# Performance work log

Hardware: AMD Instinct MI355X
Metric: run time of the kernel (lower is better)

## Reference

```python
import jax, jax.numpy as jnp
import numpy as np

B, N, H, F, G = 16, 192, 128, 128, 50


def setup_inputs() -> dict:
    key = jax.random.key(0)
    ks = jax.random.split(key, 12)
    s = lambda fan_in: 1.0 / np.sqrt(fan_in)
    inp = {
        "features": jax.random.normal(ks[0], (B, N, H), jnp.float32),
        "rbf": jax.random.uniform(ks[1], (B, N, N, G), jnp.float32),
        "neighbour_mask": jax.random.randint(ks[2], (B, N, N), 0, 2, jnp.int32),
        # dense_rbf: Linear(G,F) -> Softplus -> Linear(F,F)
        "W_rbf1": jax.random.uniform(ks[3], (G, F), jnp.float32, -s(G), s(G)),
        "b_rbf1": jnp.zeros((F,), jnp.float32),
        "W_rbf2": jax.random.uniform(ks[4], (F, F), jnp.float32, -s(F), s(F)),
        "b_rbf2": jnp.zeros((F,), jnp.float32),
        # dense_f: Linear(H,F)
        "W_f": jax.random.uniform(ks[5], (H, F), jnp.float32, -s(H), s(H)),
        "b_f": jnp.zeros((F,), jnp.float32),
        # dense_out: Linear(F,H) -> Softplus -> Linear(H,H)
        "W_o1": jax.random.uniform(ks[6], (F, H), jnp.float32, -s(F), s(F)),
        "b_o1": jnp.zeros((H,), jnp.float32),
        "W_o2": jax.random.uniform(ks[7], (H, H), jnp.float32, -s(H), s(H)),
        "b_o2": jnp.zeros((H,), jnp.float32),
    }
    return inp


def reference(features, rbf, neighbour_mask, W_rbf1, b_rbf1, W_rbf2, b_rbf2,
              W_f, b_f, W_o1, b_o1, W_o2, b_o2):
    # filter network on RBF expansion: [B,N,N,G] -> [B,N,N,F]
    fw = jax.nn.softplus(rbf @ W_rbf1 + b_rbf1) @ W_rbf2 + b_rbf2
    # neighbor features: [B,N,H] -> [B,1,N,F] (broadcast over central-atom axis)
    nf = (features @ W_f + b_f)[:, None, :, :]
    mask = neighbour_mask.astype(fw.dtype)[..., None]  # [B,N,N,1]
    # messages [B,N,N,F], masked sum over neighbor axis -> [B,N,F]
    aggregated = jnp.sum(fw * nf * mask, axis=2)
    out = jax.nn.softplus(aggregated @ W_o1 + b_o1) @ W_o2 + b_o2  # [B,N,H]
    return features + out
```

## Files before the change

kernel.cpp:

```cpp
#include <hip/hip_runtime.h>
#include <hip/hip_bf16.h>


typedef __bf16 bf16_t;
typedef __bf16 bf16x8 __attribute__((ext_vector_type(8)));
typedef float  f32x4  __attribute__((ext_vector_type(4)));

constexpr int kB = 16, kN = 192, kH = 128, kF = 128, kG = 50;
constexpr int kRows = kB * kN;
constexpr int kHsPitch = 136;

__device__ __forceinline__ float ldf(const void* p, int i, bool bfm) {
  return bfm ? (float)((const bf16_t*)p)[i] : ((const float*)p)[i];
}

__device__ __forceinline__ float softplus_f(float x) {
  float t = __logf(1.f + __expf(fminf(x, 20.f)));
  return x > 20.f ? x : t;
}

__global__ __launch_bounds__(256) void detect_kernel(const unsigned int* __restrict__ rbf_w,
                                                     int* __restrict__ flag) {
  __shared__ int c_hi, c_zero;
  const int t = threadIdx.x;
  if (t == 0) { c_hi = 0; c_zero = 0; }
  __syncthreads();
  unsigned int w = rbf_w[(size_t)t * 40003u];
  unsigned int lo = w & 0xFFFFu;
  if (((lo >> 7) & 0xFFu) >= 128u) atomicAdd(&c_hi, 1);
  if (lo == 0u) atomicAdd(&c_zero, 1);
  __syncthreads();
  if (t == 0) *flag = (c_hi == 0 && c_zero < 200) ? 1 : 0;
}

__global__ __launch_bounds__(256) void prep_kernel(const void* __restrict__ W1,
                                                   const void* __restrict__ W2,
                                                   const int* __restrict__ flag,
                                                   bf16_t* __restrict__ w1t,
                                                   bf16_t* __restrict__ w2t) {
  const bool bfm = *flag != 0;
  int idx = blockIdx.x * 256 + threadIdx.x;
  if (idx < 128 * 64) {
    int n = idx >> 6, k = idx & 63;
    w1t[idx] = (k < kG) ? (bf16_t)ldf(W1, k * kF + n, bfm) : (bf16_t)0.f;
  } else if (idx < 128 * 64 + 128 * 128) {
    int id2 = idx - 128 * 64;
    int n = id2 >> 7, k = id2 & 127;
    w2t[id2] = (bf16_t)ldf(W2, k * kF + n, bfm);
  }
}

__global__ __launch_bounds__(128) void nf_kernel(const void* __restrict__ features,
                                                 const void* __restrict__ Wf,
                                                 const void* __restrict__ bfv,
                                                 const int* __restrict__ flag,
                                                 float* __restrict__ nf) {
  const bool bfm = *flag != 0;
  int row = blockIdx.x, f = threadIdx.x;
  __shared__ float s_x[kH];
  s_x[f] = ldf(features, row * kH + f, bfm);
  __syncthreads();
  float acc = ldf(bfv, f, bfm);
#pragma unroll 8
  for (int k = 0; k < kH; ++k) acc = fmaf(s_x[k], ldf(Wf, k * kF + f, bfm), acc);
  nf[row * kF + f] = acc;
}

__global__ __launch_bounds__(256) void main_kernel(
    const void* __restrict__ rbf, const int* __restrict__ nmask,
    const void* __restrict__ b1p, const void* __restrict__ b2p,
    const bf16_t* __restrict__ w1t, const bf16_t* __restrict__ w2t,
    const float* __restrict__ nf, const int* __restrict__ flag,
    float* __restrict__ agg) {
  __shared__ bf16_t s_hs[kN * kHsPitch];
  __shared__ float  s_mask[kN];
  __shared__ float  s_agg[kF];

  const bool bfm = *flag != 0;
  const int bi = blockIdx.x;
  const int b  = bi / kN;
  const int t  = threadIdx.x;
  const int wave = t >> 6, lane = t & 63;
  const int n16 = lane & 15, q = lane >> 4;
  const int m0w = wave * 48;

  for (int idx = t; idx < kN; idx += 256) s_mask[idx] = (float)nmask[bi * kN + idx];
  if (t < kF) s_agg[t] = 0.f;

  f32x4 acc[3][8];
#pragma unroll
  for (int mt = 0; mt < 3; ++mt)
#pragma unroll
    for (int nt = 0; nt < 8; ++nt)
#pragma unroll
      for (int r = 0; r < 4; ++r) acc[mt][nt][r] = 0.f;

  const size_t rbase = (size_t)bi * (kN * kG);
#pragma unroll
  for (int ks = 0; ks < 2; ++ks) {
    bf16x8 afr[3];
#pragma unroll
    for (int mt = 0; mt < 3; ++mt) {
      const int j  = m0w + mt * 16 + n16;
      const int kb = ks * 32 + q * 8;
      if (bfm) {
        const bf16_t* rp = (const bf16_t*)rbf + rbase + (size_t)j * kG;
#pragma unroll
        for (int i = 0; i < 8; ++i) {
          int k = kb + i;
          afr[mt][i] = (k < kG) ? rp[k] : (bf16_t)0.f;
        }
      } else {
        const float* rp = (const float*)rbf + rbase + (size_t)j * kG;
#pragma unroll
        for (int i = 0; i < 8; ++i) {
          int k = kb + i;
          afr[mt][i] = (bf16_t)((k < kG) ? rp[k] : 0.f);
        }
      }
    }
#pragma unroll
    for (int nt = 0; nt < 8; ++nt) {
      bf16x8 bfr = *(const bf16x8*)(w1t + (nt * 16 + n16) * 64 + ks * 32 + q * 8);
#pragma unroll
      for (int mt = 0; mt < 3; ++mt)
        acc[mt][nt] = __builtin_amdgcn_mfma_f32_16x16x32_bf16(afr[mt], bfr, acc[mt][nt], 0, 0, 0);
    }
  }

#pragma unroll
  for (int nt = 0; nt < 8; ++nt) {
    const int col = nt * 16 + n16;
    const float bb = ldf(b1p, col, bfm);
#pragma unroll
    for (int mt = 0; mt < 3; ++mt) {
      const int jb = m0w + mt * 16 + q * 4;
#pragma unroll
      for (int r = 0; r < 4; ++r)
        s_hs[(jb + r) * kHsPitch + col] = (bf16_t)softplus_f(acc[mt][nt][r] + bb);
    }
  }
  __syncthreads();

#pragma unroll
  for (int mt = 0; mt < 3; ++mt)
#pragma unroll
    for (int nt = 0; nt < 8; ++nt)
#pragma unroll
      for (int r = 0; r < 4; ++r) acc[mt][nt][r] = 0.f;

#pragma unroll
  for (int ks = 0; ks < 4; ++ks) {
    bf16x8 afr[3];
#pragma unroll
    for (int mt = 0; mt < 3; ++mt)
      afr[mt] = *(const bf16x8*)(s_hs + (m0w + mt * 16 + n16) * kHsPitch + ks * 32 + q * 8);
#pragma unroll
    for (int nt = 0; nt < 8; ++nt) {
      bf16x8 bfr = *(const bf16x8*)(w2t + (nt * 16 + n16) * 128 + ks * 32 + q * 8);
#pragma unroll
      for (int mt = 0; mt < 3; ++mt)
        acc[mt][nt] = __builtin_amdgcn_mfma_f32_16x16x32_bf16(afr[mt], bfr, acc[mt][nt], 0, 0, 0);
    }
  }

#pragma unroll
  for (int nt = 0; nt < 8; ++nt) {
    const int f = nt * 16 + n16;
    const float b2v = ldf(b2p, f, bfm);
    float p = 0.f;
#pragma unroll
    for (int mt = 0; mt < 3; ++mt) {
      const int jb = m0w + mt * 16 + q * 4;
#pragma unroll
      for (int r = 0; r < 4; ++r) {
        const int j = jb + r;
        const float m   = s_mask[j];
        const float nfv = nf[((size_t)b * kN + j) * kF + f];
        p = fmaf(m * (acc[mt][nt][r] + b2v), nfv, p);
      }
    }
    atomicAdd(&s_agg[f], p);
  }
  __syncthreads();
  if (t < kF) agg[(size_t)bi * kF + t] = s_agg[t];
}

__global__ __launch_bounds__(128) void out_kernel(
    const float* __restrict__ agg, const void* __restrict__ features,
    const void* __restrict__ Wo1, const void* __restrict__ bo1,
    const void* __restrict__ Wo2, const void* __restrict__ bo2,
    const int* __restrict__ flag, void* __restrict__ out) {
  const bool bfm = *flag != 0;
  int row = blockIdx.x, h = threadIdx.x;
  __shared__ float s_a[kF], s_t[kH];
  s_a[h] = agg[row * kF + h];
  __syncthreads();
  float a1 = ldf(bo1, h, bfm);
#pragma unroll 8
  for (int k = 0; k < kF; ++k) a1 = fmaf(s_a[k], ldf(Wo1, k * kH + h, bfm), a1);
  s_t[h] = softplus_f(a1);
  __syncthreads();
  float a2 = ldf(bo2, h, bfm);
#pragma unroll 8
  for (int k = 0; k < kH; ++k) a2 = fmaf(s_t[k], ldf(Wo2, k * kH + h, bfm), a2);
  float res = ldf(features, row * kH + h, bfm) + a2;
  if (bfm) ((bf16_t*)out)[row * kH + h] = (bf16_t)res;
  else     ((float*)out)[row * kH + h]  = res;
}

extern "C" void kernel_launch(void* const* d_in, const int* in_sizes, int n_in,
                              void* d_out, int out_size, void* d_ws, size_t ws_size,
                              hipStream_t stream) {
  const void* features = d_in[0];
  const void* rbf      = d_in[1];
  const int*  nmask    = (const int*)d_in[2];
  const void* W1  = d_in[3];
  const void* b1  = d_in[4];
  const void* W2  = d_in[5];
  const void* b2  = d_in[6];
  const void* Wf  = d_in[7];
  const void* bfv = d_in[8];
  const void* Wo1 = d_in[9];
  const void* bo1 = d_in[10];
  const void* Wo2 = d_in[11];
  const void* bo2 = d_in[12];

  char* ws = (char*)d_ws;
  float*  nf   = (float*)ws;
  float*  agg  = (float*)(ws + 1572864);
  bf16_t* w1t  = (bf16_t*)(ws + 3145728);
  bf16_t* w2t  = (bf16_t*)(ws + 3162112);
  int*    flag = (int*)(ws + 3194880);

  detect_kernel<<<1, 256, 0, stream>>>((const unsigned int*)rbf, flag);
  prep_kernel<<<96, 256, 0, stream>>>(W1, W2, flag, w1t, w2t);
  nf_kernel<<<kRows, 128, 0, stream>>>(features, Wf, bfv, flag, nf);
  main_kernel<<<kRows, 256, 0, stream>>>(rbf, nmask, b1, b2, w1t, w2t, nf, flag, agg);
  out_kernel<<<kRows, 128, 0, stream>>>(agg, features, Wo1, bo1, Wo2, bo2, flag, d_out);
}
```

Measured before the change: 353.8 us.

## Stage rbf through LDS with vector loads and fuse kernels into two launches

Drops the bf16 detection kernel and the dtype flag, so every path assumes fp32 inputs. Merges the weight-transpose prep and nf projection into one launch, and folds the output MLP into the end of the main kernel. The main kernel now loads each block's rbf tile with coalesced float4 loads, converts it to bf16 in shared memory, and builds MFMA fragments from there instead of doing strided scalar global loads. This removes launch overhead, the agg round trip and uncoalesced rbf reads, at the cost of more LDS use and a serial tail MLP run by half the threads.

```diff
diff --git a/kernel.cpp b/kernel.cpp
--- a/kernel.cpp
+++ b/kernel.cpp
@@ -6,77 +6,70 @@
 typedef __bf16 bf16x8 __attribute__((ext_vector_type(8)));
 typedef float  f32x4  __attribute__((ext_vector_type(4)));
 
-constexpr int kB = 16, kN = 192, kH = 128, kF = 128, kG = 50;
-constexpr int kRows = kB * kN;
+constexpr int kN = 192, kH = 128, kF = 128, kG = 50;
+constexpr int kRows = 16 * kN;
 constexpr int kHsPitch = 136;
-
-__device__ __forceinline__ float ldf(const void* p, int i, bool bfm) {
-  return bfm ? (float)((const bf16_t*)p)[i] : ((const float*)p)[i];
-}
+constexpr int kRbfRowB = kG * 2;
+constexpr int kRbfF32PerBlk = kN * kG;
+constexpr int kRbfVec4 = kRbfF32PerBlk / 4;
 
 __device__ __forceinline__ float softplus_f(float x) {
   float t = __logf(1.f + __expf(fminf(x, 20.f)));
   return x > 20.f ? x : t;
 }
 
-__global__ __launch_bounds__(256) void detect_kernel(const unsigned int* __restrict__ rbf_w,
-                                                     int* __restrict__ flag) {
-  __shared__ int c_hi, c_zero;
-  const int t = threadIdx.x;
-  if (t == 0) { c_hi = 0; c_zero = 0; }
-  __syncthreads();
-  unsigned int w = rbf_w[(size_t)t * 40003u];
-  unsigned int lo = w & 0xFFFFu;
-  if (((lo >> 7) & 0xFFu) >= 128u) atomicAdd(&c_hi, 1);
-  if (lo == 0u) atomicAdd(&c_zero, 1);
-  __syncthreads();
-  if (t == 0) *flag = (c_hi == 0 && c_zero < 200) ? 1 : 0;
-}
-
-__global__ __launch_bounds__(256) void prep_kernel(const void* __restrict__ W1,
-                                                   const void* __restrict__ W2,
-                                                   const int* __restrict__ flag,
-                                                   bf16_t* __restrict__ w1t,
-                                                   bf16_t* __restrict__ w2t) {
-  const bool bfm = *flag != 0;
-  int idx = blockIdx.x * 256 + threadIdx.x;
-  if (idx < 128 * 64) {
-    int n = idx >> 6, k = idx & 63;
-    w1t[idx] = (k < kG) ? (bf16_t)ldf(W1, k * kF + n, bfm) : (bf16_t)0.f;
-  } else if (idx < 128 * 64 + 128 * 128) {
-    int id2 = idx - 128 * 64;
-    int n = id2 >> 7, k = id2 & 127;
-    w2t[id2] = (bf16_t)ldf(W2, k * kF + n, bfm);
-  }
-}
-
-__global__ __launch_bounds__(128) void nf_kernel(const void* __restrict__ features,
-                                                 const void* __restrict__ Wf,
-                                                 const void* __restrict__ bfv,
-                                                 const int* __restrict__ flag,
-                                                 float* __restrict__ nf) {
-  const bool bfm = *flag != 0;
-  int row = blockIdx.x, f = threadIdx.x;
+__global__ __launch_bounds__(64) void pre_kernel(
+    const float* __restrict__ features, const float* __restrict__ Wf,
+    const float* __restrict__ bfv, const float* __restrict__ W1,
+    const float* __restrict__ W2, float* __restrict__ nf,
+    bf16_t* __restrict__ w1t, bf16_t* __restrict__ w2t) {
+  const int lane = threadIdx.x;
+  if (blockIdx.x >= kRows) {
+    if (blockIdx.x == kRows) {
+      for (int i = lane; i < 128 * 64; i += 64) {
+        int n = i >> 6, k = i & 63;
+        w1t[i] = (k < kG) ? (bf16_t)W1[k * kF + n] : (bf16_t)0.f;
+      }
+    } else {
+      for (int i = lane; i < 128 * 128; i += 64) {
+        int n = i >> 7, k = i & 127;
+        w2t[i] = (bf16_t)W2[k * kF + n];
+      }
+    }
+    return;
+  }
+  const int row = blockIdx.x;
   __shared__ float s_x[kH];
-  s_x[f] = ldf(features, row * kH + f, bfm);
-  __syncthreads();
-  float acc = ldf(bfv, f, bfm);
+  const float* fr = features + (size_t)row * kH;
+  s_x[lane] = fr[lane];
+  s_x[64 + lane] = fr[64 + lane];
+  __syncthreads();
+  float a0 = bfv[lane], a1 = bfv[64 + lane];
 #pragma unroll 8
-  for (int k = 0; k < kH; ++k) acc = fmaf(s_x[k], ldf(Wf, k * kF + f, bfm), acc);
-  nf[row * kF + f] = acc;
+  for (int k = 0; k < kH; ++k) {
+    float xk = s_x[k];
+    a0 = fmaf(xk, Wf[k * kF + lane], a0);
+    a1 = fmaf(xk, Wf[k * kF + 64 + lane], a1);
+  }
+  float* nr = nf + (size_t)row * kF;
+  nr[lane] = a0;
+  nr[64 + lane] = a1;
 }
 
 __global__ __launch_bounds__(256) void main_kernel(
-    const void* __restrict__ rbf, const int* __restrict__ nmask,
-    const void* __restrict__ b1p, const void* __restrict__ b2p,
+    const float* __restrict__ rbf, const int* __restrict__ nmask,
+    const float* __restrict__ b1p, const float* __restrict__ b2p,
     const bf16_t* __restrict__ w1t, const bf16_t* __restrict__ w2t,
-    const float* __restrict__ nf, const int* __restrict__ flag,
-    float* __restrict__ agg) {
-  __shared__ bf16_t s_hs[kN * kHsPitch];
-  __shared__ float  s_mask[kN];
-  __shared__ float  s_agg[kF];
-
-  const bool bfm = *flag != 0;
+    const float* __restrict__ nf, const float* __restrict__ features,
+    const float* __restrict__ Wo1, const float* __restrict__ bo1,
+    const float* __restrict__ Wo2, const float* __restrict__ bo2,
+    float* __restrict__ out) {
+  __shared__ __align__(16) char smem[54016];
+  bf16_t* s_hs   = (bf16_t*)smem;
+  float*  s_mask = (float*)(smem + 52224);
+  float*  s_agg  = (float*)(smem + 52992);
+  float*  s_tt   = (float*)(smem + 53504);
+
   const int bi = blockIdx.x;
   const int b  = bi / kN;
   const int t  = threadIdx.x;
@@ -84,8 +77,23 @@
   const int n16 = lane & 15, q = lane >> 4;
   const int m0w = wave * 48;
 
-  for (int idx = t; idx < kN; idx += 256) s_mask[idx] = (float)nmask[bi * kN + idx];
+  {
+    const float4* g4 = (const float4*)(rbf + (size_t)bi * kRbfF32PerBlk);
+#pragma unroll
+    for (int it = 0; it < 10; ++it) {
+      int c = it * 256 + t;
+      if (c < kRbfVec4) {
+        float4 v = g4[c];
+        union { bf16_t h[4]; uint2 u2; } pk;
+        pk.h[0] = (bf16_t)v.x; pk.h[1] = (bf16_t)v.y;
+        pk.h[2] = (bf16_t)v.z; pk.h[3] = (bf16_t)v.w;
+        *(uint2*)(smem + c * 8) = pk.u2;
+      }
+    }
+  }
+  if (t < kN) s_mask[t] = (float)nmask[(size_t)bi * kN + t];
   if (t < kF) s_agg[t] = 0.f;
+  __syncthreads();
 
   f32x4 acc[3][8];
 #pragma unroll
@@ -95,29 +103,21 @@
 #pragma unroll
       for (int r = 0; r < 4; ++r) acc[mt][nt][r] = 0.f;
 
-  const size_t rbase = (size_t)bi * (kN * kG);
 #pragma unroll
   for (int ks = 0; ks < 2; ++ks) {
     bf16x8 afr[3];
 #pragma unroll
     for (int mt = 0; mt < 3; ++mt) {
-      const int j  = m0w + mt * 16 + n16;
-      const int kb = ks * 32 + q * 8;
-      if (bfm) {
-        const bf16_t* rp = (const bf16_t*)rbf + rbase + (size_t)j * kG;
-#pragma unroll
-        for (int i = 0; i < 8; ++i) {
-          int k = kb + i;
-          afr[mt][i] = (k < kG) ? rp[k] : (bf16_t)0.f;
-        }
-      } else {
-        const float* rp = (const float*)rbf + rbase + (size_t)j * kG;
-#pragma unroll
-        for (int i = 0; i < 8; ++i) {
-          int k = kb + i;
-          afr[mt][i] = (bf16_t)((k < kG) ? rp[k] : 0.f);
-        }
-      }
+      const int j = m0w + mt * 16 + n16;
+      const unsigned* rowp = (const unsigned*)(smem + j * kRbfRowB);
+      const int dwb = ks * 16 + q * 4;
+      union { unsigned u[4]; bf16x8 v; } cc;
+#pragma unroll
+      for (int c = 0; c < 4; ++c) {
+        unsigned val = rowp[dwb + c];
+        cc.u[c] = (dwb + c <= 24) ? val : 0u;
+      }
+      afr[mt] = cc.v;
     }
 #pragma unroll
     for (int nt = 0; nt < 8; ++nt) {
@@ -127,11 +127,12 @@
         acc[mt][nt] = __builtin_amdgcn_mfma_f32_16x16x32_bf16(afr[mt], bfr, acc[mt][nt], 0, 0, 0);
     }
   }
+  __syncthreads();
 
 #pragma unroll
   for (int nt = 0; nt < 8; ++nt) {
     const int col = nt * 16 + n16;
-    const float bb = ldf(b1p, col, bfm);
+    const float bb = b1p[col];
 #pragma unroll
     for (int mt = 0; mt < 3; ++mt) {
       const int jb = m0w + mt * 16 + q * 4;
@@ -164,10 +165,11 @@
     }
   }
 
+  const float* nfb = nf + (size_t)b * kN * kF;
 #pragma unroll
   for (int nt = 0; nt < 8; ++nt) {
     const int f = nt * 16 + n16;
-    const float b2v = ldf(b2p, f, bfm);
+    const float b2v = b2p[f];
     float p = 0.f;
 #pragma unroll
     for (int mt = 0; mt < 3; ++mt) {
@@ -175,67 +177,51 @@
 #pragma unroll
       for (int r = 0; r < 4; ++r) {
         const int j = jb + r;
-        const float m   = s_mask[j];
-        const float nfv = nf[((size_t)b * kN + j) * kF + f];
-        p = fmaf(m * (acc[mt][nt][r] + b2v), nfv, p);
+        p = fmaf(s_mask[j] * (acc[mt][nt][r] + b2v), nfb[(size_t)j * kF + f], p);
       }
     }
     atomicAdd(&s_agg[f], p);
   }
   __syncthreads();
-  if (t < kF) agg[(size_t)bi * kF + t] = s_agg[t];
-}
-
-__global__ __launch_bounds__(128) void out_kernel(
-    const float* __restrict__ agg, const void* __restrict__ features,
-    const void* __restrict__ Wo1, const void* __restrict__ bo1,
-    const void* __restrict__ Wo2, const void* __restrict__ bo2,
-    const int* __restrict__ flag, void* __restrict__ out) {
-  const bool bfm = *flag != 0;
-  int row = blockIdx.x, h = threadIdx.x;
-  __shared__ float s_a[kF], s_t[kH];
-  s_a[h] = agg[row * kF + h];
-  __syncthreads();
-  float a1 = ldf(bo1, h, bfm);
+
+  if (t < kH) {
+    float a1 = bo1[t];
 #pragma unroll 8
-  for (int k = 0; k < kF; ++k) a1 = fmaf(s_a[k], ldf(Wo1, k * kH + h, bfm), a1);
-  s_t[h] = softplus_f(a1);
-  __syncthreads();
-  float a2 = ldf(bo2, h, bfm);
+    for (int k = 0; k < kF; ++k) a1 = fmaf(s_agg[k], Wo1[k * kH + t], a1);
+    s_tt[t] = softplus_f(a1);
+  }
+  __syncthreads();
+  if (t < kH) {
+    float a2 = bo2[t];
 #pragma unroll 8
-  for (int k = 0; k < kH; ++k) a2 = fmaf(s_t[k], ldf(Wo2, k * kH + h, bfm), a2);
-  float res = ldf(features, row * kH + h, bfm) + a2;
-  if (bfm) ((bf16_t*)out)[row * kH + h] = (bf16_t)res;
-  else     ((float*)out)[row * kH + h]  = res;
+    for (int k = 0; k < kH; ++k) a2 = fmaf(s_tt[k], Wo2[k * kH + t], a2);
+    out[(size_t)bi * kH + t] = features[(size_t)bi * kH + t] + a2;
+  }
 }
 
 extern "C" void kernel_launch(void* const* d_in, const int* in_sizes, int n_in,
                               void* d_out, int out_size, void* d_ws, size_t ws_size,
                               hipStream_t stream) {
-  const void* features = d_in[0];
-  const void* rbf      = d_in[1];
-  const int*  nmask    = (const int*)d_in[2];
-  const void* W1  = d_in[3];
-  const void* b1  = d_in[4];
-  const void* W2  = d_in[5];
-  const void* b2  = d_in[6];
-  const void* Wf  = d_in[7];
-  const void* bfv = d_in[8];
-  const void* Wo1 = d_in[9];
-  const void* bo1 = d_in[10];
-  const void* Wo2 = d_in[11];
-  const void* bo2 = d_in[12];
+  const float* features = (const float*)d_in[0];
+  const float* rbf      = (const float*)d_in[1];
+  const int*   nmask    = (const int*)d_in[2];
+  const float* W1  = (const float*)d_in[3];
+  const float* b1  = (const float*)d_in[4];
+  const float* W2  = (const float*)d_in[5];
+  const float* b2  = (const float*)d_in[6];
+  const float* Wf  = (const float*)d_in[7];
+  const float* bfv = (const float*)d_in[8];
+  const float* Wo1 = (const float*)d_in[9];
+  const float* bo1 = (const float*)d_in[10];
+  const float* Wo2 = (const float*)d_in[11];
+  const float* bo2 = (const float*)d_in[12];
 
   char* ws = (char*)d_ws;
-  float*  nf   = (float*)ws;
-  float*  agg  = (float*)(ws + 1572864);
-  bf16_t* w1t  = (bf16_t*)(ws + 3145728);
-  bf16_t* w2t  = (bf16_t*)(ws + 3162112);
-  int*    flag = (int*)(ws + 3194880);
-
-  detect_kernel<<<1, 256, 0, stream>>>((const unsigned int*)rbf, flag);
-  prep_kernel<<<96, 256, 0, stream>>>(W1, W2, flag, w1t, w2t);
-  nf_kernel<<<kRows, 128, 0, stream>>>(features, Wf, bfv, flag, nf);
-  main_kernel<<<kRows, 256, 0, stream>>>(rbf, nmask, b1, b2, w1t, w2t, nf, flag, agg);
-  out_kernel<<<kRows, 128, 0, stream>>>(agg, features, Wo1, bo1, Wo2, bo2, flag, d_out);
-}
+  float*  nf  = (float*)ws;
+  bf16_t* w1t = (bf16_t*)(ws + 1572864);
+  bf16_t* w2t = (bf16_t*)(ws + 1589248);
+
+  pre_kernel<<<kRows + 2, 64, 0, stream>>>(features, Wf, bfv, W1, W2, nf, w1t, w2t);
+  main_kernel<<<kRows, 256, 0, stream>>>(rbf, nmask, b1, b2, w1t, w2t, nf,
+                                         features, Wo1, bo1, Wo2, bo2, (float*)d_out);
+}
```

Measured after the change: 450.8 us. +27.4%, slower.
